# Optimization experiments

Measured on AMD Instinct MI355X. Metric: run time of the kernel, lower is better.

Reference implementation:

```python
import jax, jax.numpy as jnp
import numpy as np
import math

B, S, H = 8, 1024, 1024
LN_EPS = 1e-5  # assumed epsilon of create_normalization_layer('layer_norm')


def setup_inputs() -> dict:
    key = jax.random.key(0)
    ks = jax.random.split(key, 6)
    context = jax.random.normal(ks[0], (B, S, H), dtype=jnp.float32)
    mask = jnp.ones((B, 1, S), dtype=jnp.int32)
    prior = jax.random.uniform(ks[1], (B, S, S), dtype=jnp.float32)
    # LayerNorm params
    gamma = jnp.ones((H,), dtype=jnp.float32)
    beta = jnp.zeros((H,), dtype=jnp.float32)
    # Dense projections (Glorot-like init)
    scale = 1.0 / np.sqrt(H)
    Wk = jax.random.normal(ks[2], (H, H), dtype=jnp.float32) * scale
    bk = jnp.zeros((H,), dtype=jnp.float32)
    Wq = jax.random.normal(ks[3], (H, H), dtype=jnp.float32) * scale
    bq = jnp.zeros((H,), dtype=jnp.float32)
    return {"context": context, "mask": mask, "prior": prior,
            "gamma": gamma, "beta": beta, "Wk": Wk, "bk": bk, "Wq": Wq, "bq": bq}


def reference(context, mask, prior, gamma, beta, Wk, bk, Wq, bq):
    dtype = context.dtype
    s = context.shape[1]
    hs = context.shape[2]
    i = jnp.arange(s)
    adj_upper = i[:, None] == (i[None, :] - 1)          # [S,S] superdiagonal
    adj_lower = i[:, None] == (i[None, :] + 1)          # subdiagonal
    adj_mask = adj_upper | adj_lower
    pad = mask[:, 0, :].astype(bool)                    # [B,S]
    pad2d = pad[:, :, None] & pad[:, None, :]           # [B,S,S]
    final_adj = adj_mask[None, :, :] & pad2d

    # LayerNorm over last axis
    mu = jnp.mean(context, axis=-1, keepdims=True)
    var = jnp.mean(jnp.square(context - mu), axis=-1, keepdims=True)
    cn = (context - mu) * jax.lax.rsqrt(var + LN_EPS) * gamma + beta

    k = cn @ Wk + bk                                    # [B,S,H]
    q = cn @ Wq + bq
    scores = jnp.einsum('bsh,bth->bst', q, k) / math.sqrt(hs)
    scores = jnp.where(final_adj, scores, jnp.asarray(-1e9, dtype))
    neibor = jax.nn.softmax(scores, axis=-1)
    neibor = jnp.sqrt(neibor * jnp.swapaxes(neibor, 1, 2) + 1e-9)
    neibor = prior + (1.0 - prior) * neibor

    triu = i[None, :] >= i[:, None]                     # [S,S] upper incl diag
    tri = triu.astype(dtype)
    b_eye = jnp.eye(s, dtype=bool)

    t = jnp.log(neibor + 1e-9)
    t = jnp.where(adj_upper[None, :, :], t, jnp.asarray(0.0, dtype))
    t = jnp.einsum('bij,jk->bik', t, tri)               # cumulative over cols
    g = jnp.exp(jnp.einsum('ij,bjk->bik', tri, t))      # hierarchical prefix product
    keep = jnp.logical_not(jnp.logical_xor(triu, b_eye))
    g = jnp.where(keep[None, :, :], g, jnp.asarray(0.0, dtype))
    neibor_diag = jnp.where(b_eye[None, :, :], jnp.asarray(1e-9, dtype), neibor)
    g = g + jnp.swapaxes(g, 1, 2) + neibor_diag
    g = g / (jnp.sum(g, axis=-1, keepdims=True) + 1e-9)

    f2d = pad2d.astype(dtype)
    g = g * f2d
    neibor = neibor * f2d
    return g, neibor
```

## Files before the change

### kernel.cpp

```cpp
#include <hip/hip_runtime.h>
#include <hip/hip_bf16.h>

#define SB 8
#define SS 1024
#define SH 1024
#define LN_EPS 1e-5f

typedef unsigned short u16;
typedef __attribute__((ext_vector_type(8))) short bf16x8;
typedef __attribute__((ext_vector_type(4))) float f32x4;

__device__ __forceinline__ u16 f2bf(float f) {
  __hip_bfloat16 h = __float2bfloat16(f);
  return *reinterpret_cast<u16*>(&h);
}
__device__ __forceinline__ float bf2f(u16 x) {
  unsigned v = ((unsigned)x) << 16;
  return __builtin_bit_cast(float, v);
}

__device__ __forceinline__ void gld16(const void* g, void* l) {
  __builtin_amdgcn_global_load_lds(
      (const __attribute__((address_space(1))) void*)g,
      (__attribute__((address_space(3))) void*)l, 16, 0, 0);
}

__global__ __launch_bounds__(256) void prep(const float* __restrict__ x,
                                            const float* __restrict__ gamma,
                                            const float* __restrict__ beta,
                                            const float* __restrict__ Wq,
                                            const float* __restrict__ Wk,
                                            const float* __restrict__ bq,
                                            u16* __restrict__ cnb,
                                            u16* __restrict__ Wq_bf,
                                            u16* __restrict__ Wk_bf,
                                            float* __restrict__ wkbq,
                                            float* __restrict__ du,
                                            float* __restrict__ dd) {
  __shared__ float p1[4], p2[4];
  const int blk = blockIdx.x;
  const int t = threadIdx.x;
  const int wave = t >> 6, lane = t & 63;

  if (blk < SB * SS) {
    const float* xr = x + (size_t)blk * SH;
    float4 v = *(const float4*)(xr + 4 * t);

    float s = v.x + v.y + v.z + v.w;
#pragma unroll
    for (int off = 32; off > 0; off >>= 1) s += __shfl_down(s, off, 64);
    if (lane == 0) p1[wave] = s;
    __syncthreads();
    const float mu = (p1[0] + p1[1] + p1[2] + p1[3]) * (1.0f / SH);

    float d0 = v.x - mu, d1 = v.y - mu, d2 = v.z - mu, d3 = v.w - mu;
    float ss = d0 * d0 + d1 * d1 + d2 * d2 + d3 * d3;
#pragma unroll
    for (int off = 32; off > 0; off >>= 1) ss += __shfl_down(ss, off, 64);
    if (lane == 0) p2[wave] = ss;
    __syncthreads();
    const float rstd =
        rsqrtf((p2[0] + p2[1] + p2[2] + p2[3]) * (1.0f / SH) + LN_EPS);

    float4 gm = *(const float4*)(gamma + 4 * t);
    float4 bt = *(const float4*)(beta + 4 * t);
    ushort4 o;
    o.x = f2bf(d0 * rstd * gm.x + bt.x);
    o.y = f2bf(d1 * rstd * gm.y + bt.y);
    o.z = f2bf(d2 * rstd * gm.z + bt.z);
    o.w = f2bf(d3 * rstd * gm.w + bt.w);
    *(ushort4*)(cnb + (size_t)blk * SH + 4 * t) = o;
    if (t == 0) {
      du[blk] = 0.f;
      dd[blk] = 0.f;
    }
  } else {
    const int w = blk - SB * SS;
    const bool is_q = (w < SH);
    const float* src = is_q ? (Wq + (size_t)w * SH) : (Wk + (size_t)(w - SH) * SH);
    u16* dst = is_q ? (Wq_bf + (size_t)w * SH) : (Wk_bf + (size_t)(w - SH) * SH);
    float4 v = *(const float4*)(src + 4 * t);
    ushort4 o;
    o.x = f2bf(v.x); o.y = f2bf(v.y); o.z = f2bf(v.z); o.w = f2bf(v.w);
    *(ushort4*)(dst + 4 * t) = o;
    if (!is_q) {
      float4 b = *(const float4*)(bq + 4 * t);
      float s = v.x * b.x + v.y * b.y + v.z * b.z + v.w * b.w;
#pragma unroll
      for (int off = 32; off > 0; off >>= 1) s += __shfl_down(s, off, 64);
      if (lane == 0) p1[wave] = s;
      __syncthreads();
      if (t == 0) wkbq[w - SH] = p1[0] + p1[1] + p1[2] + p1[3];
    }
  }
}

#define GK 1024
#define GN 1024

__global__ __launch_bounds__(256) void gemm_pt64(const u16* __restrict__ A,
                                                 const u16* __restrict__ Bt,
                                                 u16* __restrict__ C) {
  __shared__ u16 As[64 * 32];
  __shared__ u16 Bs[64 * 32];
  const int tid = threadIdx.x;
  const int m0 = blockIdx.y * 64;
  const int n0 = blockIdx.x * 64;
  const int wave = tid >> 6, lane = tid & 63;
  const int wn = wave * 16;
  const int l15 = lane & 15, q = lane >> 4;

  f32x4 acc[4] = {};

  const int srow = tid >> 2;
  const int scol = 8 * (tid & 3);
  const u16* gA = A + (size_t)(m0 + srow) * GK + scol;
  const u16* gB = Bt + (size_t)(n0 + srow) * GK + scol;
  u16* lA = &As[srow * 32 + scol];
  u16* lB = &Bs[srow * 32 + scol];

  for (int k0 = 0; k0 < GK; k0 += 32) {
    __syncthreads();
    gld16(gA + k0, lA);
    gld16(gB + k0, lB);
    __syncthreads();

    bf16x8 af[4];
#pragma unroll
    for (int fm = 0; fm < 4; ++fm)
      af[fm] = *(const bf16x8*)&As[(fm * 16 + l15) * 32 + q * 8];
    bf16x8 bfr = *(const bf16x8*)&Bs[(wn + l15) * 32 + q * 8];
#pragma unroll
    for (int fm = 0; fm < 4; ++fm)
      acc[fm] = __builtin_amdgcn_mfma_f32_16x16x32_bf16(af[fm], bfr, acc[fm],
                                                        0, 0, 0);
  }

#pragma unroll
  for (int fm = 0; fm < 4; ++fm) {
    const int row0 = m0 + fm * 16 + q * 4;
    const int col = n0 + wn + l15;
#pragma unroll
    for (int r = 0; r < 4; ++r)
      C[(size_t)(row0 + r) * GN + col] = f2bf(acc[fm][r]);
  }
}

#define BM 128
#define BN 128
#define BK 32
#define CNP 132

__global__ __launch_bounds__(256) void ugemm_fused(const u16* __restrict__ A,
                                                   const u16* __restrict__ Bt,
                                                   const u16* __restrict__ cnb,
                                                   const float* __restrict__ wkbq,
                                                   float* __restrict__ du,
                                                   float* __restrict__ dd) {
  __shared__ u16 As[BM * BK];
  __shared__ u16 Bs[BN * BK];
  __shared__ u16 cn_s[130 * CNP];
  const int tid = threadIdx.x;
  const int m0 = blockIdx.y * BM;
  const int n0 = blockIdx.x * BN;
  const int wave = tid >> 6, lane = tid & 63;
  const int wm = (wave & 1) * 64, wn = (wave >> 1) * 64;
  const int l15 = lane & 15, q = lane >> 4;

  f32x4 acc[4][4] = {};

  const int srow = tid >> 2;
  const int scol = 8 * (tid & 3);
  const u16* gA = A + (size_t)(m0 + srow) * GK + scol;
  const u16* gB = Bt + (size_t)(n0 + srow) * GK + scol;
  u16* lA = &As[srow * BK + scol];
  u16* lB = &Bs[srow * BK + scol];

  for (int k0 = 0; k0 < GK; k0 += BK) {
    __syncthreads();
    gld16(gA + k0, lA);
    gld16(gA + (size_t)64 * GK + k0, lA + 64 * BK);
    gld16(gB + k0, lB);
    gld16(gB + (size_t)64 * GK + k0, lB + 64 * BK);
    __syncthreads();

    bf16x8 af[4], bfr[4];
#pragma unroll
    for (int fm = 0; fm < 4; ++fm)
      af[fm] = *(const bf16x8*)&As[(wm + fm * 16 + l15) * BK + q * 8];
#pragma unroll
    for (int fn = 0; fn < 4; ++fn)
      bfr[fn] = *(const bf16x8*)&Bs[(wn + fn * 16 + l15) * BK + q * 8];
#pragma unroll
    for (int fm = 0; fm < 4; ++fm)
#pragma unroll
      for (int fn = 0; fn < 4; ++fn)
        acc[fm][fn] = __builtin_amdgcn_mfma_f32_16x16x32_bf16(
            af[fm], bfr[fn], acc[fm][fn], 0, 0, 0);
  }

  {
    const int c4 = (tid & 31) * 4;
    for (int rowi = (tid >> 5); rowi < 130; rowi += 8) {
      int gr = m0 - 1 + rowi;
      gr = max(0, min(SB * SS - 1, gr));
      *(ushort4*)&cn_s[rowi * CNP + c4] =
          *(const ushort4*)&cnb[(size_t)gr * SH + n0 + c4];
    }
  }
  __syncthreads();

  float wb[4];
#pragma unroll
  for (int fn = 0; fn < 4; ++fn) wb[fn] = wkbq[n0 + wn + fn * 16 + l15];

#pragma unroll
  for (int fm = 0; fm < 4; ++fm) {
#pragma unroll
    for (int rr = 0; rr < 4; ++rr) {
      const int lr = wm + fm * 16 + q * 4 + rr;
      const int r = m0 + lr;
      const int sl = r & (SS - 1);
      const u16* up = &cn_s[(lr + 2) * CNP + wn];
      const u16* dn = &cn_s[lr * CNP + wn];
      float sdu = 0.f, sdd = 0.f;
#pragma unroll
      for (int fn = 0; fn < 4; ++fn) {
        const int lc = fn * 16 + l15;
        const float a = acc[fm][fn][rr] + wb[fn];
        sdu += a * bf2f(up[lc]);
        sdd += a * bf2f(dn[lc]);
      }
      if (sl == SS - 1) sdu = 0.f;
      if (sl == 0) sdd = 0.f;
#pragma unroll
      for (int m = 1; m < 16; m <<= 1) {
        sdu += __shfl_xor(sdu, m, 64);
        sdd += __shfl_xor(sdd, m, 64);
      }
      if (l15 == 0) {
        atomicAdd(&du[r], sdu);
        atomicAdd(&dd[r], sdd);
      }
    }
  }
}

__device__ __forceinline__ void soft2(const float* __restrict__ du,
                                      const float* __restrict__ dd, int x,
                                      float& pu, float& pd) {
  const int sl = x & (SS - 1);
  if (sl == 0) { pu = 1.f; pd = 0.f; }
  else if (sl == SS - 1) { pu = 0.f; pd = 1.f; }
  else {
    const float a = du[x] * 0.03125f;
    const float b = dd[x] * 0.03125f;
    const float m = fmaxf(a, b);
    const float eu = __expf(a - m), ed = __expf(b - m);
    const float inv = 1.f / (eu + ed);
    pu = eu * inv;
    pd = ed * inv;
  }
}

__global__ __launch_bounds__(256) void rows_fused(const float* __restrict__ prior,
                                                  const int* __restrict__ mask,
                                                  const float* __restrict__ du,
                                                  const float* __restrict__ dd,
                                                  float* __restrict__ g_out,
                                                  float* __restrict__ ne_out) {
  const int r = blockIdx.x;
  const int b = r >> 10, i = r & (SS - 1);
  const int t = threadIdx.x;
  const int wave = t >> 6, lane = t & 63;
  const float nbz = 3.1622776601683795e-5f;

  float nb_im1 = nbz, nb_ip1 = nbz;
  if (i >= 1) {
    float pu_m, pd_m, pu_c, pd_c;
    soft2(du, dd, r - 1, pu_m, pd_m);
    soft2(du, dd, r, pu_c, pd_c);
    nb_im1 = sqrtf(pu_m * pd_c + 1e-9f);
  }
  if (i <= SS - 2) {
    float pu_c, pd_c, pu_p, pd_p;
    soft2(du, dd, r, pu_c, pd_c);
    soft2(du, dd, r + 1, pu_p, pd_p);
    nb_ip1 = sqrtf(pu_c * pd_p + 1e-9f);
  }

  const float* prow = prior + (size_t)r * SS;
  float4 pr = *(const float4*)(prow + 4 * t);
  const int* mrow = mask + b * SS;
  const float padi = (mrow[i] != 0) ? 1.f : 0.f;
  int4 mk = *(const int4*)(mrow + 4 * t);

  float ne[4], gsum = 0.f;
#pragma unroll
  for (int v = 0; v < 4; ++v) {
    const int k = 4 * t + v;
    const float p = (&pr.x)[v];
    const float nb = (k == i - 1) ? nb_im1 : (k == i + 1) ? nb_ip1 : nbz;
    const float n = p + (1.f - p) * nb;
    ne[v] = n;
    gsum += (k == i) ? (2.f + 1e-9f) : (1.f + n);
  }

  __shared__ float part[4];
#pragma unroll
  for (int off = 32; off > 0; off >>= 1) gsum += __shfl_down(gsum, off, 64);
  if (lane == 0) part[wave] = gsum;
  __syncthreads();
  const float inv = 1.f / (part[0] + part[1] + part[2] + part[3] + 1e-9f);

  float4 go, no;
#pragma unroll
  for (int v = 0; v < 4; ++v) {
    const int k = 4 * t + v;
    const float padk = ((&mk.x)[v] != 0) ? 1.f : 0.f;
    const float f2 = padi * padk;
    const float gt = (k == i) ? (2.f + 1e-9f) : (1.f + ne[v]);
    (&go.x)[v] = gt * inv * f2;
    (&no.x)[v] = ne[v] * f2;
  }
  *(float4*)(g_out + (size_t)r * SS + 4 * t) = go;
  *(float4*)(ne_out + (size_t)r * SS + 4 * t) = no;
}

extern "C" void kernel_launch(void* const* d_in, const int* in_sizes, int n_in,
                              void* d_out, int out_size, void* d_ws, size_t ws_size,
                              hipStream_t stream) {
  const float* context = (const float*)d_in[0];
  const int* mask = (const int*)d_in[1];
  const float* prior = (const float*)d_in[2];
  const float* gamma = (const float*)d_in[3];
  const float* beta = (const float*)d_in[4];
  const float* Wk = (const float*)d_in[5];
  const float* bk = (const float*)d_in[6];
  const float* Wq = (const float*)d_in[7];
  const float* bq = (const float*)d_in[8];
  (void)bk;

  float* out_g = (float*)d_out;
  float* out_n = out_g + (size_t)SB * SS * SS;

  char* ws = (char*)d_ws;
  u16* cnb = (u16*)ws;
  u16* Wq_bf = (u16*)(ws + ((size_t)16 << 20));
  u16* Wk_bf = (u16*)(ws + ((size_t)18 << 20));
  u16* PT = (u16*)(ws + ((size_t)20 << 20));
  float* wkbq = (float*)(ws + ((size_t)22 << 20));
  float* du = (float*)(ws + ((size_t)23 << 20));
  float* dd = (float*)(ws + ((size_t)24 << 20));

  prep<<<SB * SS + 2 * SH, 256, 0, stream>>>(context, gamma, beta, Wq, Wk, bq,
                                             cnb, Wq_bf, Wk_bf, wkbq, du, dd);
  gemm_pt64<<<dim3(16, 16), 256, 0, stream>>>(Wk_bf, Wq_bf, PT);
  ugemm_fused<<<dim3(8, 64), 256, 0, stream>>>(cnb, PT, cnb, wkbq, du, dd);
  rows_fused<<<SB * SS, 256, 0, stream>>>(prior, mask, du, dd, out_g, out_n);
}
```

Measured before the change: 189.5 us.

## Fuse weight conversion and PT GEMM into prep kernel; async-load cn tile with swizzle

Removes the separate bf16 weight-conversion pass and the standalone Wk·Wq^T GEMM launch. That GEMM now runs inside the prep kernel, reading fp32 weights directly and converting them to bf16 when staging into LDS. The Wk·bq dot products move to dedicated blocks, one wave per row. In ugemm_fused, the neighbor cn tile is prefetched with global_load_lds before the main loop, using an XOR-swizzled layout instead of a padded stride, so the load overlaps the GEMM. The trade-offs are fp32 loads inside the PT GEMM loop and one heterogeneous kernel whose blocks have unequal work.

```diff
diff --git a/kernel.cpp b/kernel.cpp
--- a/kernel.cpp
+++ b/kernel.cpp
@@ -18,6 +18,11 @@
   unsigned v = ((unsigned)x) << 16;
   return __builtin_bit_cast(float, v);
 }
+__device__ __forceinline__ ushort4 pack4(float a, float b, float c, float d) {
+  ushort4 o;
+  o.x = f2bf(a); o.y = f2bf(b); o.z = f2bf(c); o.w = f2bf(d);
+  return o;
+}
 
 __device__ __forceinline__ void gld16(const void* g, void* l) {
   __builtin_amdgcn_global_load_lds(
@@ -25,25 +30,26 @@
       (__attribute__((address_space(3))) void*)l, 16, 0, 0);
 }
 
-__global__ __launch_bounds__(256) void prep(const float* __restrict__ x,
-                                            const float* __restrict__ gamma,
-                                            const float* __restrict__ beta,
-                                            const float* __restrict__ Wq,
-                                            const float* __restrict__ Wk,
-                                            const float* __restrict__ bq,
-                                            u16* __restrict__ cnb,
-                                            u16* __restrict__ Wq_bf,
-                                            u16* __restrict__ Wk_bf,
-                                            float* __restrict__ wkbq,
-                                            float* __restrict__ du,
-                                            float* __restrict__ dd) {
+#define NPT 256
+#define NWB 16
+#define LNB0 (NPT + NWB)
+
+__global__ __launch_bounds__(256) void prep_pt(
+    const float* __restrict__ x, const float* __restrict__ gamma,
+    const float* __restrict__ beta, const float* __restrict__ Wq,
+    const float* __restrict__ Wk, const float* __restrict__ bq,
+    u16* __restrict__ cnb, u16* __restrict__ PT, float* __restrict__ wkbq,
+    float* __restrict__ du, float* __restrict__ dd) {
   __shared__ float p1[4], p2[4];
+  __shared__ u16 As[64 * 32];
+  __shared__ u16 Bs[64 * 32];
   const int blk = blockIdx.x;
   const int t = threadIdx.x;
   const int wave = t >> 6, lane = t & 63;
 
-  if (blk < SB * SS) {
-    const float* xr = x + (size_t)blk * SH;
+  if (blk >= LNB0) {
+    const int row = blk - LNB0;
+    const float* xr = x + (size_t)row * SH;
     float4 v = *(const float4*)(xr + 4 * t);
 
     float s = v.x + v.y + v.z + v.w;
@@ -64,92 +70,85 @@
 
     float4 gm = *(const float4*)(gamma + 4 * t);
     float4 bt = *(const float4*)(beta + 4 * t);
-    ushort4 o;
-    o.x = f2bf(d0 * rstd * gm.x + bt.x);
-    o.y = f2bf(d1 * rstd * gm.y + bt.y);
-    o.z = f2bf(d2 * rstd * gm.z + bt.z);
-    o.w = f2bf(d3 * rstd * gm.w + bt.w);
-    *(ushort4*)(cnb + (size_t)blk * SH + 4 * t) = o;
+    ushort4 o = pack4(d0 * rstd * gm.x + bt.x, d1 * rstd * gm.y + bt.y,
+                      d2 * rstd * gm.z + bt.z, d3 * rstd * gm.w + bt.w);
+    *(ushort4*)(cnb + (size_t)row * SH + 4 * t) = o;
     if (t == 0) {
-      du[blk] = 0.f;
-      dd[blk] = 0.f;
+      du[row] = 0.f;
+      dd[row] = 0.f;
+    }
+  } else if (blk < NPT) {
+    const int m0 = (blk >> 4) * 64;
+    const int n0 = (blk & 15) * 64;
+    const int wn = wave * 16;
+    const int l15 = lane & 15, q = lane >> 4;
+
+    f32x4 acc[4] = {};
+
+    const int srow = t >> 2;
+    const int scol = (t & 3) * 8;
+    const float* gA = Wk + (size_t)(m0 + srow) * SH + scol;
+    const float* gB = Wq + (size_t)(n0 + srow) * SH + scol;
+    u16* lA = &As[srow * 32 + scol];
+    u16* lB = &Bs[srow * 32 + scol];
+
+    for (int k0 = 0; k0 < SH; k0 += 32) {
+      float4 a0 = *(const float4*)(gA + k0);
+      float4 a1 = *(const float4*)(gA + k0 + 4);
+      float4 b0 = *(const float4*)(gB + k0);
+      float4 b1 = *(const float4*)(gB + k0 + 4);
+      __syncthreads();
+      *(ushort4*)lA = pack4(a0.x, a0.y, a0.z, a0.w);
+      *(ushort4*)(lA + 4) = pack4(a1.x, a1.y, a1.z, a1.w);
+      *(ushort4*)lB = pack4(b0.x, b0.y, b0.z, b0.w);
+      *(ushort4*)(lB + 4) = pack4(b1.x, b1.y, b1.z, b1.w);
+      __syncthreads();
+
+      bf16x8 af[4];
+#pragma unroll
+      for (int fm = 0; fm < 4; ++fm)
+        af[fm] = *(const bf16x8*)&As[(fm * 16 + l15) * 32 + q * 8];
+      bf16x8 bfr = *(const bf16x8*)&Bs[(wn + l15) * 32 + q * 8];
+#pragma unroll
+      for (int fm = 0; fm < 4; ++fm)
+        acc[fm] = __builtin_amdgcn_mfma_f32_16x16x32_bf16(af[fm], bfr, acc[fm],
+                                                          0, 0, 0);
+    }
+
+#pragma unroll
+    for (int fm = 0; fm < 4; ++fm) {
+      const int row0 = m0 + fm * 16 + q * 4;
+      const int col = n0 + wn + l15;
+#pragma unroll
+      for (int r = 0; r < 4; ++r)
+        PT[(size_t)(row0 + r) * SH + col] = f2bf(acc[fm][r]);
     }
   } else {
-    const int w = blk - SB * SS;
-    const bool is_q = (w < SH);
-    const float* src = is_q ? (Wq + (size_t)w * SH) : (Wk + (size_t)(w - SH) * SH);
-    u16* dst = is_q ? (Wq_bf + (size_t)w * SH) : (Wk_bf + (size_t)(w - SH) * SH);
-    float4 v = *(const float4*)(src + 4 * t);
-    ushort4 o;
-    o.x = f2bf(v.x); o.y = f2bf(v.y); o.z = f2bf(v.z); o.w = f2bf(v.w);
-    *(ushort4*)(dst + 4 * t) = o;
-    if (!is_q) {
-      float4 b = *(const float4*)(bq + 4 * t);
-      float s = v.x * b.x + v.y * b.y + v.z * b.z + v.w * b.w;
+    const int rbase = (blk - NPT) * 64 + wave * 16;
+    float4 bv[4];
+#pragma unroll
+    for (int j = 0; j < 4; ++j)
+      bv[j] = *(const float4*)(bq + lane * 16 + 4 * j);
+    for (int i = 0; i < 16; ++i) {
+      const float* wr = Wk + (size_t)(rbase + i) * SH + lane * 16;
+      float s = 0.f;
+#pragma unroll
+      for (int j = 0; j < 4; ++j) {
+        float4 w4 = *(const float4*)(wr + 4 * j);
+        s += w4.x * bv[j].x + w4.y * bv[j].y + w4.z * bv[j].z + w4.w * bv[j].w;
+      }
 #pragma unroll
       for (int off = 32; off > 0; off >>= 1) s += __shfl_down(s, off, 64);
-      if (lane == 0) p1[wave] = s;
-      __syncthreads();
-      if (t == 0) wkbq[w - SH] = p1[0] + p1[1] + p1[2] + p1[3];
+      if (lane == 0) wkbq[rbase + i] = s;
     }
   }
 }
 
 #define GK 1024
 #define GN 1024
-
-__global__ __launch_bounds__(256) void gemm_pt64(const u16* __restrict__ A,
-                                                 const u16* __restrict__ Bt,
-                                                 u16* __restrict__ C) {
-  __shared__ u16 As[64 * 32];
-  __shared__ u16 Bs[64 * 32];
-  const int tid = threadIdx.x;
-  const int m0 = blockIdx.y * 64;
-  const int n0 = blockIdx.x * 64;
-  const int wave = tid >> 6, lane = tid & 63;
-  const int wn = wave * 16;
-  const int l15 = lane & 15, q = lane >> 4;
-
-  f32x4 acc[4] = {};
-
-  const int srow = tid >> 2;
-  const int scol = 8 * (tid & 3);
-  const u16* gA = A + (size_t)(m0 + srow) * GK + scol;
-  const u16* gB = Bt + (size_t)(n0 + srow) * GK + scol;
-  u16* lA = &As[srow * 32 + scol];
-  u16* lB = &Bs[srow * 32 + scol];
-
-  for (int k0 = 0; k0 < GK; k0 += 32) {
-    __syncthreads();
-    gld16(gA + k0, lA);
-    gld16(gB + k0, lB);
-    __syncthreads();
-
-    bf16x8 af[4];
-#pragma unroll
-    for (int fm = 0; fm < 4; ++fm)
-      af[fm] = *(const bf16x8*)&As[(fm * 16 + l15) * 32 + q * 8];
-    bf16x8 bfr = *(const bf16x8*)&Bs[(wn + l15) * 32 + q * 8];
-#pragma unroll
-    for (int fm = 0; fm < 4; ++fm)
-      acc[fm] = __builtin_amdgcn_mfma_f32_16x16x32_bf16(af[fm], bfr, acc[fm],
-                                                        0, 0, 0);
-  }
-
-#pragma unroll
-  for (int fm = 0; fm < 4; ++fm) {
-    const int row0 = m0 + fm * 16 + q * 4;
-    const int col = n0 + wn + l15;
-#pragma unroll
-    for (int r = 0; r < 4; ++r)
-      C[(size_t)(row0 + r) * GN + col] = f2bf(acc[fm][r]);
-  }
-}
-
 #define BM 128
 #define BN 128
 #define BK 32
-#define CNP 132
 
 __global__ __launch_bounds__(256) void ugemm_fused(const u16* __restrict__ A,
                                                    const u16* __restrict__ Bt,
@@ -159,13 +158,28 @@
                                                    float* __restrict__ dd) {
   __shared__ u16 As[BM * BK];
   __shared__ u16 Bs[BN * BK];
-  __shared__ u16 cn_s[130 * CNP];
+  __shared__ u16 cn_s[144 * 128];
   const int tid = threadIdx.x;
   const int m0 = blockIdx.y * BM;
   const int n0 = blockIdx.x * BN;
   const int wave = tid >> 6, lane = tid & 63;
   const int wm = (wave & 1) * 64, wn = (wave >> 1) * 64;
   const int l15 = lane & 15, q = lane >> 4;
+
+  {
+    const int lr4 = lane >> 4;
+    const int cb = lane & 15;
+#pragma unroll
+    for (int rd = 0; rd < 9; ++rd) {
+      const int rowbase = rd * 16 + wave * 4;
+      const int rowi = rowbase + lr4;
+      const int sw = (rowi >> 2) & 3;
+      int gr = m0 - 1 + rowi;
+      gr = max(0, min(SB * SS - 1, gr));
+      gld16(cnb + (size_t)gr * SH + n0 + (((cb ^ (sw << 1))) << 3),
+            &cn_s[rowbase * 128]);
+    }
+  }
 
   f32x4 acc[4][4] = {};
 
@@ -199,17 +213,6 @@
             af[fm], bfr[fn], acc[fm][fn], 0, 0, 0);
   }
 
-  {
-    const int c4 = (tid & 31) * 4;
-    for (int rowi = (tid >> 5); rowi < 130; rowi += 8) {
-      int gr = m0 - 1 + rowi;
-      gr = max(0, min(SB * SS - 1, gr));
-      *(ushort4*)&cn_s[rowi * CNP + c4] =
-          *(const ushort4*)&cnb[(size_t)gr * SH + n0 + c4];
-    }
-  }
-  __syncthreads();
-
   float wb[4];
 #pragma unroll
   for (int fn = 0; fn < 4; ++fn) wb[fn] = wkbq[n0 + wn + fn * 16 + l15];
@@ -221,15 +224,18 @@
       const int lr = wm + fm * 16 + q * 4 + rr;
       const int r = m0 + lr;
       const int sl = r & (SS - 1);
-      const u16* up = &cn_s[(lr + 2) * CNP + wn];
-      const u16* dn = &cn_s[lr * CNP + wn];
+      const int ru = lr + 2;
+      const int swu = ((ru >> 2) & 3) << 4;
+      const int swd = ((lr >> 2) & 3) << 4;
+      const u16* up = &cn_s[ru * 128];
+      const u16* dn = &cn_s[lr * 128];
       float sdu = 0.f, sdd = 0.f;
 #pragma unroll
       for (int fn = 0; fn < 4; ++fn) {
-        const int lc = fn * 16 + l15;
+        const int lc = wn + fn * 16 + l15;
         const float a = acc[fm][fn][rr] + wb[fn];
-        sdu += a * bf2f(up[lc]);
-        sdd += a * bf2f(dn[lc]);
+        sdu += a * bf2f(up[lc ^ swu]);
+        sdd += a * bf2f(dn[lc ^ swd]);
       }
       if (sl == SS - 1) sdu = 0.f;
       if (sl == 0) sdd = 0.f;
@@ -346,16 +352,13 @@
 
   char* ws = (char*)d_ws;
   u16* cnb = (u16*)ws;
-  u16* Wq_bf = (u16*)(ws + ((size_t)16 << 20));
-  u16* Wk_bf = (u16*)(ws + ((size_t)18 << 20));
-  u16* PT = (u16*)(ws + ((size_t)20 << 20));
-  float* wkbq = (float*)(ws + ((size_t)22 << 20));
-  float* du = (float*)(ws + ((size_t)23 << 20));
-  float* dd = (float*)(ws + ((size_t)24 << 20));
-
-  prep<<<SB * SS + 2 * SH, 256, 0, stream>>>(context, gamma, beta, Wq, Wk, bq,
-                                             cnb, Wq_bf, Wk_bf, wkbq, du, dd);
-  gemm_pt64<<<dim3(16, 16), 256, 0, stream>>>(Wk_bf, Wq_bf, PT);
+  u16* PT = (u16*)(ws + ((size_t)16 << 20));
+  float* wkbq = (float*)(ws + ((size_t)18 << 20));
+  float* du = (float*)(ws + ((size_t)19 << 20));
+  float* dd = (float*)(ws + ((size_t)20 << 20));
+
+  prep_pt<<<LNB0 + SB * SS, 256, 0, stream>>>(context, gamma, beta, Wq, Wk, bq,
+                                              cnb, PT, wkbq, du, dd);
   ugemm_fused<<<dim3(8, 64), 256, 0, stream>>>(cnb, PT, cnb, wkbq, du, dd);
   rows_fused<<<SB * SS, 256, 0, stream>>>(prior, mask, du, dd, out_g, out_n);
 }
```

New measurement: 191.5 us. Within noise of the previous version (+1.1%).
